# Kernel optimization log

Measured on AMD Instinct MI355X. Metric: run time of the kernel, lower is better.

Reference implementation:

```python
import jax, jax.numpy as jnp
import numpy as np

N_NODES = 100000
N_EDGES = 1600000
IN_FEATS = 128
H1 = 256
H2 = 256
N_CLASSES = 64


def setup_inputs() -> dict:
    key = jax.random.key(0)
    ks = jax.random.split(key, 12)
    x = jax.random.normal(ks[0], (N_NODES, IN_FEATS), dtype=jnp.float32)
    src = jax.random.randint(ks[1], (N_EDGES,), 0, N_NODES, dtype=jnp.int64 if jax.config.jax_enable_x64 else jnp.int32)
    dst = jax.random.randint(ks[2], (N_EDGES,), 0, N_NODES, dtype=jnp.int64 if jax.config.jax_enable_x64 else jnp.int32)
    def lin(kw, kb, fan_in, fan_out):
        bound = 1.0 / np.sqrt(fan_in)
        W = jax.random.uniform(kw, (fan_out, fan_in), minval=-bound, maxval=bound, dtype=jnp.float32)
        b = jax.random.uniform(kb, (fan_out,), minval=-bound, maxval=bound, dtype=jnp.float32)
        return W, b
    W1, b1 = lin(ks[3], ks[4], 2 * IN_FEATS, H1)
    W2, b2 = lin(ks[5], ks[6], 2 * H1, H2)
    W3, b3 = lin(ks[7], ks[8], 2 * H2, N_CLASSES)
    return {"x": x, "src": src, "dst": dst,
            "W1": W1, "b1": b1, "W2": W2, "b2": b2, "W3": W3, "b3": b3}


def _sage_conv(h, src, dst, W, b):
    # message = copy from src node, reduce = mean at dst node (DGL copy_u + mean)
    m = jnp.take(h, src, axis=0)                                  # [E, d]
    s = jax.ops.segment_sum(m, dst, num_segments=N_NODES)         # [N, d]
    deg = jax.ops.segment_sum(jnp.ones((m.shape[0],), h.dtype), dst,
                              num_segments=N_NODES)               # [N]
    h_N = s / jnp.maximum(deg, 1.0)[:, None]                      # isolated nodes -> 0 (DGL behavior)
    h_total = jnp.concatenate([h, h_N], axis=1)                   # [N, 2d]
    return h_total @ W.T + b                                      # dropout inactive at eval (p=0.05)


def reference(x, src, dst, W1, b1, W2, b2, W3, b3):
    h = jax.nn.relu(_sage_conv(x, src, dst, W1, b1))
    h = jax.nn.relu(_sage_conv(h, src, dst, W2, b2))
    return _sage_conv(h, src, dst, W3, b3)
```

## Files before the change

### kernel.cpp

```cpp
#include <hip/hip_runtime.h>
#include <hip/hip_bf16.h>
#include <cstdint>
#include <cstddef>

#define N_NODES 100000
#define N_EDGES 1600000
#define NBUCK   256
#define NPB     391
#define NB_E    ((N_EDGES + 4095) / 4096)

#define FK_X    NB_E
#define FK_W1   (FK_X + 12500)
#define FK_W2   (FK_W1 + 64)
#define FK_W3   (FK_W2 + 128)
#define FK_END  (FK_W3 + 32)

typedef __attribute__((ext_vector_type(8))) short short8;
typedef __attribute__((ext_vector_type(4))) float floatx4;

__device__ inline float bf_lo(unsigned int u) { return __uint_as_float(u << 16); }
__device__ inline float bf_hi(unsigned int u) { return __uint_as_float(u & 0xffff0000u); }
__device__ inline unsigned short f2bf(float f) {
  unsigned int u = __float_as_uint(f);
  u += 0x7fffu + ((u >> 16) & 1u);
  return (unsigned short)(u >> 16);
}

__device__ inline void cvt4_body(const float* __restrict__ in,
                                 unsigned short* __restrict__ out, int t) {
  float4 v = ((const float4*)in)[t];
  ushort4 o;
  o.x = f2bf(v.x); o.y = f2bf(v.y); o.z = f2bf(v.z); o.w = f2bf(v.w);
  ((ushort4*)out)[t] = o;
}

__global__ __launch_bounds__(256)
void front_kernel(const int* __restrict__ dst, int* __restrict__ blockHist,
                  const float* __restrict__ x,  unsigned short* __restrict__ H0,
                  const float* __restrict__ W1, unsigned short* __restrict__ Wb1,
                  const float* __restrict__ W2, unsigned short* __restrict__ Wb2,
                  const float* __restrict__ W3, unsigned short* __restrict__ Wb3) {
  __shared__ int hist[NBUCK];
  const int b = blockIdx.x, tid = threadIdx.x;
  if (b < FK_X) {
    hist[tid] = 0;
    __syncthreads();
#pragma unroll
    for (int i = 0; i < 16; ++i) {
      int e = b * 4096 + i * 256 + tid;
      if (e < N_EDGES) atomicAdd(&hist[dst[e] / NPB], 1);
    }
    __syncthreads();
    blockHist[b * NBUCK + tid] = hist[tid];
  } else if (b < FK_W1) {
    cvt4_body(x, H0, (b - FK_X) * 256 + tid);
  } else if (b < FK_W2) {
    cvt4_body(W1, Wb1, (b - FK_W1) * 256 + tid);
  } else if (b < FK_W3) {
    cvt4_body(W2, Wb2, (b - FK_W2) * 256 + tid);
  } else {
    int t = (b - FK_W3) * 256 + tid;
    int idx4 = t * 4;
    int r = idx4 >> 8, c = idx4 & 255;
    float4 v = *(const float4*)(W3 + (size_t)(r & 63) * 512 + (r >> 6) * 256 + c);
    ushort4 o;
    o.x = f2bf(v.x); o.y = f2bf(v.y); o.z = f2bf(v.z); o.w = f2bf(v.w);
    *(ushort4*)(Wb3 + (size_t)r * 256 + c) = o;
  }
}

__device__ inline int wave_incl_scan(int v, int lane) {
#pragma unroll
  for (int off = 1; off < 64; off <<= 1) {
    int t = __shfl_up(v, off, 64);
    if (lane >= off) v += t;
  }
  return v;
}

__global__ __launch_bounds__(256)
void scanB1_kernel(const int* __restrict__ blockHist,
                   int* __restrict__ blockOfs, int* __restrict__ bucketCount) {
  int bucket = (int)((blockIdx.x * 256 + threadIdx.x) >> 6);
  if (bucket >= NBUCK) return;
  int lane = threadIdx.x & 63;
  int carry = 0;
  for (int c0 = 0; c0 < NB_E; c0 += 64) {
    int blk = c0 + lane;
    int v = (blk < NB_E) ? blockHist[blk * NBUCK + bucket] : 0;
    int incl = wave_incl_scan(v, lane);
    if (blk < NB_E) blockOfs[blk * NBUCK + bucket] = carry + incl - v;
    carry += __shfl(incl, 63, 64);
  }
  if (lane == 63) bucketCount[bucket] = carry;
}

__global__ void scanB2_kernel(const int* __restrict__ bucketCount,
                              int* __restrict__ bucketBase) {
  __shared__ int wsum[4];
  int t = threadIdx.x, lane = t & 63, wid = t >> 6;
  int v = bucketCount[t];
  int incl = wave_incl_scan(v, lane);
  if (lane == 63) wsum[wid] = incl;
  __syncthreads();
  int off = 0;
  for (int w = 0; w < wid; ++w) off += wsum[w];
  bucketBase[t] = off + incl - v;
  if (t == NBUCK - 1) bucketBase[NBUCK] = off + incl;
}

__global__ __launch_bounds__(256)
void pass1b_kernel(const int* __restrict__ src, const int* __restrict__ dst,
                   const int* __restrict__ blockOfs, const int* __restrict__ bucketBase,
                   unsigned int* __restrict__ staging) {
  __shared__ int hist[NBUCK];
  hist[threadIdx.x] = bucketBase[threadIdx.x] + blockOfs[blockIdx.x * NBUCK + threadIdx.x];
  __syncthreads();
#pragma unroll
  for (int i = 0; i < 16; ++i) {
    int e = blockIdx.x * 4096 + i * 256 + threadIdx.x;
    if (e < N_EDGES) {
      int d = dst[e];
      int b = d / NPB;
      int pos = atomicAdd(&hist[b], 1);
      staging[pos] = (unsigned)src[e] | ((unsigned)(d - b * NPB) << 17);
    }
  }
}

__global__ __launch_bounds__(512)
void pass2_kernel(const unsigned int* __restrict__ staging, const int* __restrict__ bucketBase,
                  int* __restrict__ start, float* __restrict__ invdeg,
                  int* __restrict__ esrc) {
  __shared__ int cnt[512];
  __shared__ int cur[512];
  __shared__ int wsum[8];
  const int b = blockIdx.x, tid = threadIdx.x;
  const int lane = tid & 63, wid = tid >> 6;
  const int n0 = b * NPB, n1 = min(n0 + NPB, N_NODES);
  const int nLocal = n1 - n0;
  const int p0 = bucketBase[b], p1 = bucketBase[b + 1];

  cnt[tid] = 0;
  __syncthreads();
  for (int e = p0 + tid; e < p1; e += 512)
    atomicAdd(&cnt[staging[e] >> 17], 1);
  __syncthreads();

  int c = cnt[tid];
  int incl = wave_incl_scan(c, lane);
  if (lane == 63) wsum[wid] = incl;
  __syncthreads();
  if (wid == 0) {
    int v = (lane < 8) ? wsum[lane] : 0;
    int i2 = wave_incl_scan(v, lane);
    if (lane < 8) wsum[lane] = i2 - v;
  }
  __syncthreads();
  int excl = wsum[wid] + incl - c;
  cur[tid] = excl;
  if (tid < nLocal) {
    start[n0 + tid] = p0 + excl;
    invdeg[n0 + tid] = 1.0f / fmaxf((float)c, 1.0f);
  }
  if (b == NBUCK - 1 && tid == 0) start[N_NODES] = N_EDGES;
  __syncthreads();

  for (int e = p0 + tid; e < p1; e += 512) {
    unsigned int pr = staging[e];
    int pos = p0 + atomicAdd(&cur[pr >> 17], 1);
    esrc[pos] = (int)(pr & 0x1FFFFu);
  }
}

template<int D>
__global__ __launch_bounds__(256)
void gather_mean(const unsigned short* __restrict__ h,
                 const int* __restrict__ start,
                 const int* __restrict__ esrc,
                 const float* __restrict__ invdeg,
                 unsigned short* __restrict__ hn) {
  int wave = (int)((blockIdx.x * 256 + threadIdx.x) >> 6);
  if (wave >= N_NODES) return;
  int lane = threadIdx.x & 63;
  int s0 = start[wave], s1 = start[wave + 1];
  constexpr int FPL = D / 64;
  float acc[FPL] = {};
  const unsigned short* base = h + lane * FPL;

  int e = s0;
  if constexpr (FPL == 4) {
    for (; e + 4 <= s1; e += 4) {
      int sn0 = esrc[e], sn1 = esrc[e + 1], sn2 = esrc[e + 2], sn3 = esrc[e + 3];
      uint2 p0 = *(const uint2*)(base + (size_t)sn0 * D);
      uint2 p1 = *(const uint2*)(base + (size_t)sn1 * D);
      uint2 p2 = *(const uint2*)(base + (size_t)sn2 * D);
      uint2 p3 = *(const uint2*)(base + (size_t)sn3 * D);
      acc[0] += bf_lo(p0.x) + bf_lo(p1.x) + bf_lo(p2.x) + bf_lo(p3.x);
      acc[1] += bf_hi(p0.x) + bf_hi(p1.x) + bf_hi(p2.x) + bf_hi(p3.x);
      acc[2] += bf_lo(p0.y) + bf_lo(p1.y) + bf_lo(p2.y) + bf_lo(p3.y);
      acc[3] += bf_hi(p0.y) + bf_hi(p1.y) + bf_hi(p2.y) + bf_hi(p3.y);
    }
    for (; e < s1; ++e) {
      int sn = esrc[e];
      uint2 p = *(const uint2*)(base + (size_t)sn * D);
      acc[0] += bf_lo(p.x); acc[1] += bf_hi(p.x);
      acc[2] += bf_lo(p.y); acc[3] += bf_hi(p.y);
    }
  } else {
    for (; e + 4 <= s1; e += 4) {
      int sn0 = esrc[e], sn1 = esrc[e + 1], sn2 = esrc[e + 2], sn3 = esrc[e + 3];
      unsigned int p0 = *(const unsigned int*)(base + (size_t)sn0 * D);
      unsigned int p1 = *(const unsigned int*)(base + (size_t)sn1 * D);
      unsigned int p2 = *(const unsigned int*)(base + (size_t)sn2 * D);
      unsigned int p3 = *(const unsigned int*)(base + (size_t)sn3 * D);
      acc[0] += bf_lo(p0) + bf_lo(p1) + bf_lo(p2) + bf_lo(p3);
      acc[1] += bf_hi(p0) + bf_hi(p1) + bf_hi(p2) + bf_hi(p3);
    }
    for (; e < s1; ++e) {
      int sn = esrc[e];
      unsigned int p = *(const unsigned int*)(base + (size_t)sn * D);
      acc[0] += bf_lo(p); acc[1] += bf_hi(p);
    }
  }

  float inv = invdeg[wave];
  unsigned short* out = hn + (size_t)wave * D + lane * FPL;
  if constexpr (FPL == 4) {
    ushort4 o;
    o.x = f2bf(acc[0] * inv); o.y = f2bf(acc[1] * inv);
    o.z = f2bf(acc[2] * inv); o.w = f2bf(acc[3] * inv);
    *(ushort4*)out = o;
  } else {
    ushort2 o;
    o.x = f2bf(acc[0] * inv); o.y = f2bf(acc[1] * inv);
    *(ushort2*)out = o;
  }
}

__global__ __launch_bounds__(256)
void gather_add64(const unsigned short* __restrict__ Y3,
                  const int* __restrict__ start, const int* __restrict__ esrc,
                  const float* __restrict__ invdeg, float* __restrict__ out) {
  int wave = (int)((blockIdx.x * 256 + threadIdx.x) >> 6);
  if (wave >= N_NODES) return;
  int lane = threadIdx.x & 63;
  int slot = lane >> 4, l16 = lane & 15;
  int s0 = start[wave], s1 = start[wave + 1];
  const unsigned short* ybase = Y3 + 4 * l16;
  float a0 = 0.f, a1 = 0.f, a2 = 0.f, a3 = 0.f;
  int e = s0 + slot;
  for (; e + 12 < s1; e += 16) {
    int sn0 = esrc[e], sn1 = esrc[e + 4], sn2 = esrc[e + 8], sn3 = esrc[e + 12];
    uint2 p0 = *(const uint2*)(ybase + (size_t)sn0 * 64);
    uint2 p1 = *(const uint2*)(ybase + (size_t)sn1 * 64);
    uint2 p2 = *(const uint2*)(ybase + (size_t)sn2 * 64);
    uint2 p3 = *(const uint2*)(ybase + (size_t)sn3 * 64);
    a0 += bf_lo(p0.x) + bf_lo(p1.x) + bf_lo(p2.x) + bf_lo(p3.x);
    a1 += bf_hi(p0.x) + bf_hi(p1.x) + bf_hi(p2.x) + bf_hi(p3.x);
    a2 += bf_lo(p0.y) + bf_lo(p1.y) + bf_lo(p2.y) + bf_lo(p3.y);
    a3 += bf_hi(p0.y) + bf_hi(p1.y) + bf_hi(p2.y) + bf_hi(p3.y);
  }
  for (; e < s1; e += 4) {
    uint2 p = *(const uint2*)(ybase + (size_t)esrc[e] * 64);
    a0 += bf_lo(p.x); a1 += bf_hi(p.x);
    a2 += bf_lo(p.y); a3 += bf_hi(p.y);
  }
  a0 += __shfl_xor(a0, 16, 64); a1 += __shfl_xor(a1, 16, 64);
  a2 += __shfl_xor(a2, 16, 64); a3 += __shfl_xor(a3, 16, 64);
  a0 += __shfl_xor(a0, 32, 64); a1 += __shfl_xor(a1, 32, 64);
  a2 += __shfl_xor(a2, 32, 64); a3 += __shfl_xor(a3, 32, 64);
  if (slot == 0) {
    float inv = invdeg[wave];
    float4* q = (float4*)(out + (size_t)wave * 64 + 4 * l16);
    float4 v = *q;
    v.x += inv * a0; v.y += inv * a1; v.z += inv * a2; v.w += inv * a3;
    *q = v;
  }
}

template<int D, int DOUT, int BN, bool RELU, bool OUTF32, int MODE>
__global__ __launch_bounds__(256)
void sage_gemm(const unsigned short* __restrict__ H,
               const unsigned short* __restrict__ HN,
               const unsigned short* __restrict__ Wb,
               const float* __restrict__ bias,
               void* __restrict__ outp,
               unsigned short* __restrict__ y3) {
  constexpr int K   = (MODE == 1) ? D : 2 * D;
  constexpr int BM  = 128, KC = 32;
  constexpr int NCHUNK = K / KC;
  constexpr int AF  = BM / 16;
  constexpr int BF  = BN / 16;
  constexpr int FR  = AF + BF;
  constexpr int NMF = 4;
  constexpr int NJF = BF / 2;

  __shared__ __align__(16) unsigned short lds0[FR * 512];
  __shared__ __align__(16) unsigned short lds1[FR * 512];

  const int tid  = threadIdx.x;
  const int wave = tid >> 6, lane = tid & 63;
  const int l16  = lane & 15, quad = lane >> 4;
  const int n0   = blockIdx.x * BM;
  const int bn0  = blockIdx.y * BN;
  const int wm   = wave >> 1, wn = wave & 1;

  floatx4 acc[NMF][NJF] = {};

  auto stage = [&](int c, unsigned short* buf) {
    const int kc = c * KC;
    const unsigned short* srcH = (kc < D) ? H : HN;
    const int kb = (kc < D) ? kc : kc - D;
    const int w0 = __builtin_amdgcn_readfirstlane(wave);
#pragma unroll
    for (int i = 0; i < FR / 4; ++i) {
      const int fu = w0 + 4 * i;
      const unsigned short* g;
      if (fu < AF) {
        int row = min(n0 + fu * 16 + l16, N_NODES - 1);
        g = srcH + (size_t)row * D + kb + quad * 8;
      } else {
        int col = bn0 + (fu - AF) * 16 + l16;
        g = Wb + (size_t)col * K + kc + quad * 8;
      }
      __builtin_amdgcn_global_load_lds(
          (const __attribute__((address_space(1))) unsigned int*)g,
          (__attribute__((address_space(3))) unsigned int*)(buf + fu * 512),
          16, 0, 0);
    }
  };

  auto compute = [&](const unsigned short* buf) {
    short8 b[NJF];
#pragma unroll
    for (int jt = 0; jt < NJF; ++jt)
      b[jt] = *(const short8*)(buf + (AF + wn * NJF + jt) * 512 + lane * 8);
#pragma unroll
    for (int mi = 0; mi < NMF; ++mi) {
      short8 a = *(const short8*)(buf + (wm * NMF + mi) * 512 + lane * 8);
#pragma unroll
      for (int jt = 0; jt < NJF; ++jt)
        acc[mi][jt] = __builtin_amdgcn_mfma_f32_16x16x32_bf16(a, b[jt], acc[mi][jt], 0, 0, 0);
    }
  };

  stage(0, lds0);
  __syncthreads();
#pragma unroll 1
  for (int c = 0; c < NCHUNK; c += 2) {
    stage(c + 1, lds1);
    compute(lds0);
    __syncthreads();
    if (c + 2 < NCHUNK) stage(c + 2, lds0);
    compute(lds1);
    __syncthreads();
  }

#pragma unroll
  for (int mi = 0; mi < NMF; ++mi) {
#pragma unroll
    for (int jt = 0; jt < NJF; ++jt) {
      int j = bn0 + wn * (NJF * 16) + jt * 16 + l16;
      float bj = (MODE == 1 && wn == 1) ? 0.0f : bias[j];
#pragma unroll
      for (int r = 0; r < 4; ++r) {
        int node = n0 + wm * 64 + mi * 16 + quad * 4 + r;
        if (node < N_NODES) {
          float v = acc[mi][jt][r];
          if constexpr (MODE == 1) {
            if (wn == 0) ((float*)outp)[(size_t)node * 64 + j] = v + bj;
            else y3[(size_t)node * 64 + (j - 64)] = f2bf(v);
          } else {
            v += bj;
            if (RELU) v = fmaxf(v, 0.0f);
            if (OUTF32) ((float*)outp)[(size_t)node * DOUT + j] = v;
            else ((unsigned short*)outp)[(size_t)node * DOUT + j] = f2bf(v);
          }
        }
      }
    }
  }
}

extern "C" void kernel_launch(void* const* d_in, const int* in_sizes, int n_in,
                              void* d_out, int out_size, void* d_ws, size_t ws_size,
                              hipStream_t stream) {
  const float* x   = (const float*)d_in[0];
  const int*   src = (const int*)d_in[1];
  const int*   dst = (const int*)d_in[2];
  const float* W1 = (const float*)d_in[3];
  const float* b1 = (const float*)d_in[4];
  const float* W2 = (const float*)d_in[5];
  const float* b2 = (const float*)d_in[6];
  const float* W3 = (const float*)d_in[7];
  const float* b3 = (const float*)d_in[8];

  char* ws = (char*)d_ws;
  unsigned short* H0 = (unsigned short*)ws; ws += (size_t)N_NODES * 128 * 2;
  unsigned short* H1 = (unsigned short*)ws; ws += (size_t)N_NODES * 256 * 2;
  unsigned short* H2 = (unsigned short*)ws; ws += (size_t)N_NODES * 256 * 2;
  unsigned short* HN = (unsigned short*)ws; ws += (size_t)N_NODES * 256 * 2;
  unsigned int* staging = (unsigned int*)ws; ws += (size_t)N_EDGES * 4;
  int* esrc   = (int*)ws;  ws += (size_t)N_EDGES * 4;
  int* startp = (int*)ws;  ws += (size_t)(N_NODES + 32) * 4;
  float* invdeg = (float*)ws; ws += (size_t)(N_NODES + 32) * 4;
  int* bucketBase  = (int*)ws; ws += (NBUCK + 32) * 4;
  int* bucketCount = (int*)ws; ws += NBUCK * 4;
  int* blockHist   = (int*)ws; ws += (size_t)NB_E * NBUCK * 4;
  int* blockOfs    = (int*)ws; ws += (size_t)NB_E * NBUCK * 4;
  unsigned short* Y3 = (unsigned short*)ws; ws += (size_t)N_NODES * 64 * 2;
  unsigned short* Wb1 = (unsigned short*)ws; ws += 256 * 256 * 2;
  unsigned short* Wb2 = (unsigned short*)ws; ws += 256 * 512 * 2;
  unsigned short* Wb3 = (unsigned short*)ws; ws += 128 * 256 * 2;

  front_kernel<<<FK_END, 256, 0, stream>>>(dst, blockHist, x, H0, W1, Wb1, W2, Wb2, W3, Wb3);
  scanB1_kernel<<<(NBUCK * 64 + 255) / 256, 256, 0, stream>>>(blockHist, blockOfs, bucketCount);
  scanB2_kernel<<<1, NBUCK, 0, stream>>>(bucketCount, bucketBase);
  pass1b_kernel<<<NB_E, 256, 0, stream>>>(src, dst, blockOfs, bucketBase, staging);
  pass2_kernel<<<NBUCK, 512, 0, stream>>>(staging, bucketBase, startp, invdeg, esrc);

  const int GGRID = (N_NODES * 64 + 255) / 256;
  const int MG = (N_NODES + 127) / 128;

  gather_mean<128><<<GGRID, 256, 0, stream>>>(H0, startp, esrc, invdeg, HN);
  sage_gemm<128, 256, 128, true, false, 0><<<dim3(MG, 2), 256, 0, stream>>>(H0, HN, Wb1, b1, H1, nullptr);

  gather_mean<256><<<GGRID, 256, 0, stream>>>(H1, startp, esrc, invdeg, HN);
  sage_gemm<256, 256, 128, true, false, 0><<<dim3(MG, 2), 256, 0, stream>>>(H1, HN, Wb2, b2, H2, nullptr);

  sage_gemm<256, 128, 128, false, true, 1><<<dim3(MG, 1), 256, 0, stream>>>(H2, nullptr, Wb3, b3, (float*)d_out, Y3);
  gather_add64<<<GGRID, 256, 0, stream>>>(Y3, startp, esrc, invdeg, (float*)d_out);
}
```

Before: 556.2 us.

## Move dtype conversions into scatter pass and widen GEMM N-tile to full output

The bf16 conversions of x and the weights move out of the histogram kernel and into the scatter (pass1b) kernel, so they run alongside the scatter work instead of the histogram work. The layer-1 and layer-2 GEMMs now use a 256-wide N tile with a 1D grid, so each block computes all output columns. This avoids loading the A tiles (H and HN) twice. The trade-off is half as many blocks and likely more registers or LDS per block.

```diff
diff --git a/kernel.cpp b/kernel.cpp
--- a/kernel.cpp
+++ b/kernel.cpp
@@ -9,11 +9,11 @@
 #define NPB     391
 #define NB_E    ((N_EDGES + 4095) / 4096)
 
-#define FK_X    NB_E
-#define FK_W1   (FK_X + 12500)
-#define FK_W2   (FK_W1 + 64)
-#define FK_W3   (FK_W2 + 128)
-#define FK_END  (FK_W3 + 32)
+#define MID_P   NB_E
+#define MID_X   (MID_P + 12500)
+#define MID_W1  (MID_X + 64)
+#define MID_W2  (MID_W1 + 128)
+#define MID_END (MID_W2 + 32)
 
 typedef __attribute__((ext_vector_type(8))) short short8;
 typedef __attribute__((ext_vector_type(4))) float floatx4;
@@ -35,38 +35,18 @@
 }
 
 __global__ __launch_bounds__(256)
-void front_kernel(const int* __restrict__ dst, int* __restrict__ blockHist,
-                  const float* __restrict__ x,  unsigned short* __restrict__ H0,
-                  const float* __restrict__ W1, unsigned short* __restrict__ Wb1,
-                  const float* __restrict__ W2, unsigned short* __restrict__ Wb2,
-                  const float* __restrict__ W3, unsigned short* __restrict__ Wb3) {
+void pass1a_kernel(const int* __restrict__ dst, int* __restrict__ blockHist) {
   __shared__ int hist[NBUCK];
   const int b = blockIdx.x, tid = threadIdx.x;
-  if (b < FK_X) {
-    hist[tid] = 0;
-    __syncthreads();
-#pragma unroll
-    for (int i = 0; i < 16; ++i) {
-      int e = b * 4096 + i * 256 + tid;
-      if (e < N_EDGES) atomicAdd(&hist[dst[e] / NPB], 1);
-    }
-    __syncthreads();
-    blockHist[b * NBUCK + tid] = hist[tid];
-  } else if (b < FK_W1) {
-    cvt4_body(x, H0, (b - FK_X) * 256 + tid);
-  } else if (b < FK_W2) {
-    cvt4_body(W1, Wb1, (b - FK_W1) * 256 + tid);
-  } else if (b < FK_W3) {
-    cvt4_body(W2, Wb2, (b - FK_W2) * 256 + tid);
-  } else {
-    int t = (b - FK_W3) * 256 + tid;
-    int idx4 = t * 4;
-    int r = idx4 >> 8, c = idx4 & 255;
-    float4 v = *(const float4*)(W3 + (size_t)(r & 63) * 512 + (r >> 6) * 256 + c);
-    ushort4 o;
-    o.x = f2bf(v.x); o.y = f2bf(v.y); o.z = f2bf(v.z); o.w = f2bf(v.w);
-    *(ushort4*)(Wb3 + (size_t)r * 256 + c) = o;
-  }
+  hist[tid] = 0;
+  __syncthreads();
+#pragma unroll
+  for (int i = 0; i < 16; ++i) {
+    int e = b * 4096 + i * 256 + tid;
+    if (e < N_EDGES) atomicAdd(&hist[dst[e] / NPB], 1);
+  }
+  __syncthreads();
+  blockHist[b * NBUCK + tid] = hist[tid];
 }
 
 __device__ inline int wave_incl_scan(int v, int lane) {
@@ -110,21 +90,42 @@
 }
 
 __global__ __launch_bounds__(256)
-void pass1b_kernel(const int* __restrict__ src, const int* __restrict__ dst,
-                   const int* __restrict__ blockOfs, const int* __restrict__ bucketBase,
-                   unsigned int* __restrict__ staging) {
+void mid_kernel(const int* __restrict__ src, const int* __restrict__ dst,
+                const int* __restrict__ blockOfs, const int* __restrict__ bucketBase,
+                unsigned int* __restrict__ staging,
+                const float* __restrict__ x,  unsigned short* __restrict__ H0,
+                const float* __restrict__ W1, unsigned short* __restrict__ Wb1,
+                const float* __restrict__ W2, unsigned short* __restrict__ Wb2,
+                const float* __restrict__ W3, unsigned short* __restrict__ Wb3) {
   __shared__ int hist[NBUCK];
-  hist[threadIdx.x] = bucketBase[threadIdx.x] + blockOfs[blockIdx.x * NBUCK + threadIdx.x];
-  __syncthreads();
-#pragma unroll
-  for (int i = 0; i < 16; ++i) {
-    int e = blockIdx.x * 4096 + i * 256 + threadIdx.x;
-    if (e < N_EDGES) {
-      int d = dst[e];
-      int b = d / NPB;
-      int pos = atomicAdd(&hist[b], 1);
-      staging[pos] = (unsigned)src[e] | ((unsigned)(d - b * NPB) << 17);
-    }
+  const int b = blockIdx.x, tid = threadIdx.x;
+  if (b < MID_P) {
+    hist[tid] = bucketBase[tid] + blockOfs[b * NBUCK + tid];
+    __syncthreads();
+#pragma unroll
+    for (int i = 0; i < 16; ++i) {
+      int e = b * 4096 + i * 256 + tid;
+      if (e < N_EDGES) {
+        int d = dst[e];
+        int bb = d / NPB;
+        int pos = atomicAdd(&hist[bb], 1);
+        staging[pos] = (unsigned)src[e] | ((unsigned)(d - bb * NPB) << 17);
+      }
+    }
+  } else if (b < MID_X) {
+    cvt4_body(x, H0, (b - MID_P) * 256 + tid);
+  } else if (b < MID_W1) {
+    cvt4_body(W1, Wb1, (b - MID_X) * 256 + tid);
+  } else if (b < MID_W2) {
+    cvt4_body(W2, Wb2, (b - MID_W1) * 256 + tid);
+  } else {
+    int t = (b - MID_W2) * 256 + tid;
+    int idx4 = t * 4;
+    int r = idx4 >> 8, c = idx4 & 255;
+    float4 v = *(const float4*)(W3 + (size_t)(r & 63) * 512 + (r >> 6) * 256 + c);
+    ushort4 o;
+    o.x = f2bf(v.x); o.y = f2bf(v.y); o.z = f2bf(v.z); o.w = f2bf(v.w);
+    *(ushort4*)(Wb3 + (size_t)r * 256 + c) = o;
   }
 }
 
@@ -414,21 +415,22 @@
   unsigned short* Wb2 = (unsigned short*)ws; ws += 256 * 512 * 2;
   unsigned short* Wb3 = (unsigned short*)ws; ws += 128 * 256 * 2;
 
-  front_kernel<<<FK_END, 256, 0, stream>>>(dst, blockHist, x, H0, W1, Wb1, W2, Wb2, W3, Wb3);
+  pass1a_kernel<<<NB_E, 256, 0, stream>>>(dst, blockHist);
   scanB1_kernel<<<(NBUCK * 64 + 255) / 256, 256, 0, stream>>>(blockHist, blockOfs, bucketCount);
   scanB2_kernel<<<1, NBUCK, 0, stream>>>(bucketCount, bucketBase);
-  pass1b_kernel<<<NB_E, 256, 0, stream>>>(src, dst, blockOfs, bucketBase, staging);
+  mid_kernel<<<MID_END, 256, 0, stream>>>(src, dst, blockOfs, bucketBase, staging,
+                                          x, H0, W1, Wb1, W2, Wb2, W3, Wb3);
   pass2_kernel<<<NBUCK, 512, 0, stream>>>(staging, bucketBase, startp, invdeg, esrc);
 
   const int GGRID = (N_NODES * 64 + 255) / 256;
   const int MG = (N_NODES + 127) / 128;
 
   gather_mean<128><<<GGRID, 256, 0, stream>>>(H0, startp, esrc, invdeg, HN);
-  sage_gemm<128, 256, 128, true, false, 0><<<dim3(MG, 2), 256, 0, stream>>>(H0, HN, Wb1, b1, H1, nullptr);
+  sage_gemm<128, 256, 256, true, false, 0><<<MG, 256, 0, stream>>>(H0, HN, Wb1, b1, H1, nullptr);
 
   gather_mean<256><<<GGRID, 256, 0, stream>>>(H1, startp, esrc, invdeg, HN);
-  sage_gemm<256, 256, 128, true, false, 0><<<dim3(MG, 2), 256, 0, stream>>>(H1, HN, Wb2, b2, H2, nullptr);
-
-  sage_gemm<256, 128, 128, false, true, 1><<<dim3(MG, 1), 256, 0, stream>>>(H2, nullptr, Wb3, b3, (float*)d_out, Y3);
+  sage_gemm<256, 256, 256, true, false, 0><<<MG, 256, 0, stream>>>(H1, HN, Wb2, b2, H2, nullptr);
+
+  sage_gemm<256, 128, 128, false, true, 1><<<MG, 256, 0, stream>>>(H2, nullptr, Wb3, b3, (float*)d_out, Y3);
   gather_add64<<<GGRID, 256, 0, stream>>>(Y3, startp, esrc, invdeg, (float*)d_out);
 }
```

Measured after the change: 610.9 us. +9.8%, slower.
